# Kernel tuning notes

Hardware: AMD Instinct MI355X
Metric: run time of the kernel (lower is better)

## Reference

```python
import jax, jax.numpy as jnp
import numpy as np

B, T, C = 4, 2048, 1024
N_HEAD = 16
HEAD_DIM = C // N_HEAD


def setup_inputs() -> dict:
    key = jax.random.key(0)
    k1, k2, k3 = jax.random.split(key, 3)
    scale = 1.0 / np.sqrt(C)
    return {
        "x": jax.random.normal(k1, (B, T, C), dtype=jnp.float32),
        "W_attn": jax.random.normal(k2, (C, 3 * C), dtype=jnp.float32) * scale,
        "b_attn": jnp.zeros((3 * C,), dtype=jnp.float32),
        "W_proj": jax.random.normal(k3, (C, C), dtype=jnp.float32) * scale,
        "b_proj": jnp.zeros((C,), dtype=jnp.float32),
    }


def reference(x, W_attn, b_attn, W_proj, b_proj):
    Bt, Tt, Ct = x.shape
    qkv = x @ W_attn + b_attn                      # [B,T,3C]
    q, k, v = jnp.split(qkv, 3, axis=-1)
    # [B,T,C] -> [B,H,T,D]
    def heads(t):
        return t.reshape(Bt, Tt, N_HEAD, HEAD_DIM).transpose(0, 2, 1, 3)
    q, k, v = heads(q), heads(k), heads(v)
    att = jnp.einsum("bhqd,bhkd->bhqk", q, k) * (1.0 / np.sqrt(HEAD_DIM))
    causal = jnp.tril(jnp.ones((Tt, Tt), dtype=bool))
    att = jnp.where(causal, att, jnp.finfo(att.dtype).min)
    att = jax.nn.softmax(att, axis=-1)
    # dropout = 0.0 (eval mode): identity
    y = jnp.einsum("bhqk,bhkd->bhqd", att, v)      # [B,H,T,D]
    y = y.transpose(0, 2, 1, 3).reshape(Bt, Tt, Ct)
    return y @ W_proj + b_proj
```

## Files before the change

kernel.cpp:

```cpp
#include <hip/hip_runtime.h>
#include <hip/hip_bf16.h>
#include <cstdint>

#define B_SZ 4
#define T_SZ 2048
#define C_SZ 1024
#define H_SZ 16
#define D_SZ 64
#define BT_SZ (B_SZ * T_SZ)
#define C3_SZ (3 * C_SZ)
#define NKC (C_SZ / 32)

typedef __attribute__((ext_vector_type(8))) short bf16x8;
typedef __attribute__((ext_vector_type(4))) float f32x4;
typedef __attribute__((ext_vector_type(4))) unsigned short ushort4v;
typedef __attribute__((ext_vector_type(4))) unsigned int uint4v;

typedef __attribute__((address_space(3))) unsigned int lds_u32;
typedef __attribute__((address_space(1))) const unsigned int glb_u32;

__device__ __forceinline__ unsigned short f2bf(float f) {
  unsigned u = __builtin_bit_cast(unsigned, f);
  u += 0x7fffu + ((u >> 16) & 1u);
  return (unsigned short)(u >> 16);
}

__device__ __forceinline__ unsigned packbf2(float lo, float hi) {
  return __builtin_amdgcn_perm(__builtin_bit_cast(unsigned, hi),
                               __builtin_bit_cast(unsigned, lo), 0x07060302u);
}

__device__ __forceinline__ void gll16(const unsigned short* g,
                                      unsigned short* l) {
  __builtin_amdgcn_global_load_lds((glb_u32*)g, (lds_u32*)l, 16, 0, 0);
}


__device__ __forceinline__ void pack_x_task(const float* __restrict__ x,
                                            unsigned short* __restrict__ Af,
                                            int task, int lane) {
  const int quad = lane >> 4, n = lane & 15;
  const int tb = task >> 5, kc = task & 31;
  const float* src = x + (size_t)(tb * 16 + n) * C_SZ + kc * 32 + quad * 8;
  float4 a = *(const float4*)src;
  float4 b = *(const float4*)(src + 4);
  ushort4v o0, o1;
  o0[0] = f2bf(a.x); o0[1] = f2bf(a.y); o0[2] = f2bf(a.z); o0[3] = f2bf(a.w);
  o1[0] = f2bf(b.x); o1[1] = f2bf(b.y); o1[2] = f2bf(b.z); o1[3] = f2bf(b.w);
  unsigned short* dst = Af + ((size_t)((tb * NKC + kc) * 4 + quad) * 16 + n) * 8;
  *(ushort4v*)dst = o0;
  *(ushort4v*)(dst + 4) = o1;
}

__device__ __forceinline__ void pack_w_task(const float* __restrict__ W,
                                            unsigned short* __restrict__ Wb,
                                            int N, int task, int lane) {
  const int quad = lane >> 4, n = lane & 15;
  const int nt = task >> 5, kc = task & 31;
  const int col = nt * 16 + n;
  const int k0 = kc * 32 + quad * 8;
  ushort4v o0, o1;
#pragma unroll
  for (int i = 0; i < 4; ++i) o0[i] = f2bf(W[(size_t)(k0 + i) * N + col]);
#pragma unroll
  for (int i = 0; i < 4; ++i) o1[i] = f2bf(W[(size_t)(k0 + 4 + i) * N + col]);
  unsigned short* dst = Wb + ((size_t)((nt * NKC + kc) * 4 + quad) * 16 + n) * 8;
  *(ushort4v*)dst = o0;
  *(ushort4v*)(dst + 4) = o1;
}

__global__ __launch_bounds__(256) void pack_all(
    const float* __restrict__ x, const float* __restrict__ Wa,
    const float* __restrict__ Wp, unsigned short* __restrict__ Af,
    unsigned short* __restrict__ Wab, unsigned short* __restrict__ Wpb) {
  const int bx = blockIdx.x;
  const int sub = threadIdx.x >> 6;
  const int lane = threadIdx.x & 63;
  if (bx < 4096) {
    pack_x_task(x, Af, bx * 4 + sub, lane);
  } else if (bx < 4096 + 1536) {
    pack_w_task(Wa, Wab, C3_SZ, (bx - 4096) * 4 + sub, lane);
  } else {
    pack_w_task(Wp, Wpb, C_SZ, (bx - 5632) * 4 + sub, lane);
  }
}

__device__ __forceinline__ void gemm128_mainloop(
    const unsigned short* __restrict__ A, const unsigned short* __restrict__ B,
    int tbB, int ntB, unsigned short* smem, f32x4 acc[4][4]) {
  const int tid = threadIdx.x;
  const int w = tid >> 6, lane = tid & 63;
  const int quad = lane >> 4, n = lane & 15;
  const int wr = w >> 1, wc = w & 1;
  unsigned short* smemA = smem;
  unsigned short* smemB = smem + 8192;

  for (int kc0 = 0; kc0 < NKC; kc0 += 2) {
#pragma unroll
    for (int i2 = 0; i2 < 2; ++i2) {
      const int i = 2 * w + i2;
      const unsigned short* gA =
          A + ((size_t)(tbB + i) * NKC + kc0) * 512 + lane * 8;
      const unsigned short* gB =
          B + ((size_t)(ntB + i) * NKC + kc0) * 512 + lane * 8;
      gll16(gA, smemA + i * 1024);
      gll16(gA + 512, smemA + i * 1024 + 512);
      gll16(gB, smemB + i * 1024);
      gll16(gB + 512, smemB + i * 1024 + 512);
    }
    __syncthreads();
#pragma unroll
    for (int kcl = 0; kcl < 2; ++kcl) {
      bf16x8 af[4], bfr[4];
#pragma unroll
      for (int m = 0; m < 4; ++m)
        af[m] = *(const bf16x8*)(smemA + (wr * 4 + m) * 1024 +
                                 (kcl * 4 + quad) * 128 + n * 8);
#pragma unroll
      for (int nn = 0; nn < 4; ++nn)
        bfr[nn] = *(const bf16x8*)(smemB + (wc * 4 + nn) * 1024 +
                                   (kcl * 4 + quad) * 128 + n * 8);
#pragma unroll
      for (int m = 0; m < 4; ++m)
#pragma unroll
        for (int nn = 0; nn < 4; ++nn)
          acc[m][nn] = __builtin_amdgcn_mfma_f32_16x16x32_bf16(
              af[m], bfr[nn], acc[m][nn], 0, 0, 0);
    }
    __syncthreads();
  }
}

__global__ __launch_bounds__(256) void qkv_mfma(
    const unsigned short* __restrict__ Af, const unsigned short* __restrict__ Wab,
    const float* __restrict__ bias, unsigned short* __restrict__ Qf,
    unsigned short* __restrict__ Kf, unsigned short* __restrict__ Vf,
    int by0) {
  __shared__ unsigned short smem[16384];
  const int tid = threadIdx.x;
  const int w = tid >> 6, lane = tid & 63;
  const int quad = lane >> 4, n = lane & 15;
  const int wr = w >> 1, wc = w & 1;
  const int f = blockIdx.x;
  const int xcd = f & 7, i = f >> 3;
  const int by = by0 + xcd * 4 + (i / 24);
  const int bx = i % 24;
  f32x4 acc[4][4];
#pragma unroll
  for (int m = 0; m < 4; ++m)
#pragma unroll
    for (int nn = 0; nn < 4; ++nn) acc[m][nn] = (f32x4){0.f, 0.f, 0.f, 0.f};

  gemm128_mainloop(Af, Wab, by * 8, bx * 8, smem, acc);

  const int cb = bx * 128 + wc * 64;
  const int which = cb >> 10;
  const int h = (cb & 1023) >> 6;
  const int gr0 = by * 128 + wr * 64;
  const int b = gr0 >> 11;
  const int t0 = gr0 & 2047;
  const size_t bhoff = (size_t)(b * H_SZ + h) * (T_SZ * D_SZ);
  float bfl[4];
#pragma unroll
  for (int nn = 0; nn < 4; ++nn) bfl[nn] = bias[cb + nn * 16 + n];

  if (which < 2) {
    unsigned short* dst = ((which == 0) ? Qf : Kf) + bhoff;
    const float scl = (which == 0) ? 0.18033688f : 1.0f;
#pragma unroll
    for (int m = 0; m < 4; ++m) {
      const int tb = (t0 + m * 16) >> 4;
#pragma unroll
      for (int nn = 0; nn < 4; ++nn) {
        const int dc = nn >> 1;
        const int qd = (nn & 1) * 2 + (n >> 3);
        const int jq = n & 7;
#pragma unroll
        for (int r = 0; r < 4; ++r) {
          const int nq = quad * 4 + r;
          dst[((size_t)((tb * 2 + dc) * 4 + qd)) * 128 + nq * 8 + jq] =
              f2bf((acc[m][nn][r] + bfl[nn]) * scl);
        }
      }
    }
  } else {
    unsigned short* dst = Vf + bhoff;
    const int gb0 = t0 >> 5;
#pragma unroll
    for (int m = 0; m < 4; ++m) {
      const int gb = gb0 + (m >> 1);
#pragma unroll
      for (int nn = 0; nn < 4; ++nn) {
        ushort4v o;
#pragma unroll
        for (int r = 0; r < 4; ++r) o[r] = f2bf(acc[m][nn][r] + bfl[nn]);
        *(ushort4v*)(dst + ((size_t)((gb * 4 + nn) * 4 + quad)) * 128 +
                     n * 8 + (m & 1) * 4) = o;
      }
    }
  }
}

__global__ __launch_bounds__(256) void proj_mfma(
    const unsigned short* __restrict__ Yf, const unsigned short* __restrict__ Wpb,
    const float* __restrict__ bias, float* __restrict__ out) {
  __shared__ unsigned short smem[16384];
  const int tid = threadIdx.x;
  const int w = tid >> 6, lane = tid & 63;
  const int quad = lane >> 4, n = lane & 15;
  const int wr = w >> 1, wc = w & 1;
  const int f = blockIdx.x;
  const int xcd = f & 7, i = f >> 3;
  const int by = xcd * 8 + (i / 8);
  const int bx = i % 8;
  f32x4 acc[4][4];
#pragma unroll
  for (int m = 0; m < 4; ++m)
#pragma unroll
    for (int nn = 0; nn < 4; ++nn) acc[m][nn] = (f32x4){0.f, 0.f, 0.f, 0.f};

  gemm128_mainloop(Yf, Wpb, by * 8, bx * 8, smem, acc);

  const int cb = bx * 128 + wc * 64;
  const int gr0 = by * 128 + wr * 64;
  float bfl[4];
#pragma unroll
  for (int nn = 0; nn < 4; ++nn) bfl[nn] = bias[cb + nn * 16 + n];
#pragma unroll
  for (int m = 0; m < 4; ++m)
#pragma unroll
    for (int nn = 0; nn < 4; ++nn)
#pragma unroll
      for (int r = 0; r < 4; ++r)
        out[(size_t)(gr0 + m * 16 + quad * 4 + r) * C_SZ + cb + nn * 16 + n] =
            acc[m][nn][r] + bfl[nn];
}

__global__ __launch_bounds__(64) void attn_mfma(
    const unsigned short* __restrict__ Qf,
    const unsigned short* __restrict__ Kf,
    const unsigned short* __restrict__ Vf, unsigned short* __restrict__ Yf) {
  const int lane = threadIdx.x;
  const int quad = lane >> 4;
  const int n = lane & 15;
  const int bx = blockIdx.x;
  const int qt = 31 - (bx >> 6);
  const int bh = bx & 63;
  const int b = bh >> 4, h = bh & 15;
  const int wq0 = qt * 64;
  const size_t bhoff = (size_t)bh * (T_SZ * D_SZ);
  const bf16x8* Qp = (const bf16x8*)(Qf + bhoff);
  const bf16x8* Kp = (const bf16x8*)(Kf + bhoff);
  const bf16x8* Vp = (const bf16x8*)(Vf + bhoff);

  bf16x8 qfr[4][2];
#pragma unroll
  for (int m = 0; m < 4; ++m) {
    const int tb = (wq0 >> 4) + m;
#pragma unroll
    for (int dc = 0; dc < 2; ++dc)
      qfr[m][dc] = Qp[((tb * 2 + dc) * 4 + quad) * 16 + n];
  }

  bf16x8 kfr[4][2], vfr[2][4];
  f32x4 O[4][4];
  f32x4 ls[4];
#pragma unroll
  for (int m = 0; m < 4; ++m) {
    ls[m] = (f32x4){0.f, 0.f, 0.f, 0.f};
#pragma unroll
    for (int dv = 0; dv < 4; ++dv) O[m][dv] = (f32x4){0.f, 0.f, 0.f, 0.f};
  }

#pragma unroll
  for (int s = 0; s < 4; ++s) {
    kfr[s][0] = Kp[((s * 2 + 0) * 4 + quad) * 16 + n];
    kfr[s][1] = Kp[((s * 2 + 1) * 4 + quad) * 16 + n];
  }
#pragma unroll
  for (int g = 0; g < 2; ++g)
#pragma unroll
    for (int dv = 0; dv < 4; ++dv)
      vfr[g][dv] = Vp[((g * 4 + dv) * 4 + quad) * 16 + n];

  for (int kt = 0; kt < qt; ++kt) {
#pragma unroll
    for (int m = 0; m < 4; ++m) {
      f32x4 st[4];
#pragma unroll
      for (int s = 0; s < 4; ++s) {
        f32x4 z = {0.f, 0.f, 0.f, 0.f};
        z = __builtin_amdgcn_mfma_f32_16x16x32_bf16(kfr[s][0], qfr[m][0], z, 0, 0, 0);
        z = __builtin_amdgcn_mfma_f32_16x16x32_bf16(kfr[s][1], qfr[m][1], z, 0, 0, 0);
        st[s] = z;
      }
      if (m == 3) {
        const int tb0 = (kt + 1) * 4;
#pragma unroll
        for (int s = 0; s < 4; ++s) {
          kfr[s][0] = Kp[(((tb0 + s) * 2 + 0) * 4 + quad) * 16 + n];
          kfr[s][1] = Kp[(((tb0 + s) * 2 + 1) * 4 + quad) * 16 + n];
        }
      }
      uint4v pw[2];
#pragma unroll
      for (int s = 0; s < 4; ++s) {
        float pr[4];
#pragma unroll
        for (int r = 0; r < 4; ++r) {
          pr[r] = __builtin_amdgcn_exp2f(st[s][r]);
          ls[m][r] += pr[r];
        }
        pw[s >> 1][(s & 1) * 2 + 0] = packbf2(pr[0], pr[1]);
        pw[s >> 1][(s & 1) * 2 + 1] = packbf2(pr[2], pr[3]);
      }
#pragma unroll
      for (int g = 0; g < 2; ++g) {
        const bf16x8 pg = __builtin_bit_cast(bf16x8, pw[g]);
#pragma unroll
        for (int dv = 0; dv < 4; ++dv)
          O[m][dv] = __builtin_amdgcn_mfma_f32_16x16x32_bf16(
              pg, vfr[g][dv], O[m][dv], 0, 0, 0);
      }
      if (m == 3) {
        const int gb0 = (kt + 1) * 2;
#pragma unroll
        for (int g = 0; g < 2; ++g)
#pragma unroll
          for (int dv = 0; dv < 4; ++dv)
            vfr[g][dv] = Vp[(((gb0 + g) * 4 + dv) * 4 + quad) * 16 + n];
      }
    }
  }

  {
#pragma unroll
    for (int m = 0; m < 4; ++m) {
      f32x4 st[4];
#pragma unroll
      for (int s = 0; s < 4; ++s) {
        f32x4 z = {0.f, 0.f, 0.f, 0.f};
        if (s <= m) {
          z = __builtin_amdgcn_mfma_f32_16x16x32_bf16(kfr[s][0], qfr[m][0], z, 0, 0, 0);
          z = __builtin_amdgcn_mfma_f32_16x16x32_bf16(kfr[s][1], qfr[m][1], z, 0, 0, 0);
        }
        st[s] = z;
      }
      uint4v pw[2] = {(uint4v){0, 0, 0, 0}, (uint4v){0, 0, 0, 0}};
#pragma unroll
      for (int s = 0; s < 4; ++s) {
        if (s <= m) {
          float pr[4];
#pragma unroll
          for (int r = 0; r < 4; ++r) {
            float v = st[s][r];
            if (s == m && quad * 4 + r > n) v = -1e30f;
            pr[r] = __builtin_amdgcn_exp2f(v);
            ls[m][r] += pr[r];
          }
          pw[s >> 1][(s & 1) * 2 + 0] = packbf2(pr[0], pr[1]);
          pw[s >> 1][(s & 1) * 2 + 1] = packbf2(pr[2], pr[3]);
        }
      }
#pragma unroll
      for (int g = 0; g < 2; ++g) {
        if (g * 2 <= m) {
          const bf16x8 pg = __builtin_bit_cast(bf16x8, pw[g]);
#pragma unroll
          for (int dv = 0; dv < 4; ++dv)
            O[m][dv] = __builtin_amdgcn_mfma_f32_16x16x32_bf16(
                pg, vfr[g][dv], O[m][dv], 0, 0, 0);
        }
      }
    }
  }

#pragma unroll
  for (int m = 0; m < 4; ++m) {
    float lt = ls[m][0] + ls[m][1] + ls[m][2] + ls[m][3];
    lt += __shfl_xor(lt, 16);
    lt += __shfl_xor(lt, 32);
    const float inv = 1.0f / lt;
    float iv[4];
#pragma unroll
    for (int r = 0; r < 4; ++r) iv[r] = __shfl(inv, quad * 4 + r);
    const int tb = (b * T_SZ + wq0 + m * 16) >> 4;
#pragma unroll
    for (int dv = 0; dv < 4; ++dv) {
      const int kc = h * 2 + (dv >> 1);
      const int qa = (dv & 1) * 2 + (n >> 3);
      const int ja = n & 7;
#pragma unroll
      for (int r = 0; r < 4; ++r) {
        const int na = quad * 4 + r;
        Yf[((size_t)((tb * NKC + kc) * 4 + qa)) * 128 + na * 8 + ja] =
            f2bf(O[m][dv][r] * iv[r]);
      }
    }
  }
}

extern "C" void kernel_launch(void* const* d_in, const int* in_sizes, int n_in,
                              void* d_out, int out_size, void* d_ws,
                              size_t ws_size, hipStream_t stream) {
  const float* x = (const float*)d_in[0];
  const float* W_attn = (const float*)d_in[1];
  const float* b_attn = (const float*)d_in[2];
  const float* W_proj = (const float*)d_in[3];
  const float* b_proj = (const float*)d_in[4];
  float* out = (float*)d_out;

  const size_t perbf = (size_t)B_SZ * H_SZ * T_SZ * D_SZ;
  unsigned short* Af = (unsigned short*)d_ws;
  unsigned short* Wab = Af + (size_t)BT_SZ * C_SZ;
  unsigned short* Wpb = Wab + (size_t)C_SZ * C3_SZ;
  unsigned short* Qf = Wpb + (size_t)C_SZ * C_SZ;
  unsigned short* Kf = Qf + perbf;
  unsigned short* Vf = Kf + perbf;
  unsigned short* Yf = Vf + perbf;

  pack_all<<<6144, 256, 0, stream>>>(x, W_attn, W_proj, Af, Wab, Wpb);
  qkv_mfma<<<768, 256, 0, stream>>>(Af, Wab, b_attn, Qf, Kf, Vf, 0);
  qkv_mfma<<<768, 256, 0, stream>>>(Af, Wab, b_attn, Qf, Kf, Vf, 32);
  attn_mfma<<<dim3(32 * B_SZ * H_SZ), 64, 0, stream>>>(Qf, Kf, Vf, Yf);
  proj_mfma<<<512, 256, 0, stream>>>(Yf, Wpb, b_proj, out);
}
```

Measured before the change: 240.8 us.

## Pair causal query tiles per attention block and merge QKV launches

```diff
diff --git a/kernel.cpp b/kernel.cpp
--- a/kernel.cpp
+++ b/kernel.cpp
@@ -134,8 +134,7 @@
 __global__ __launch_bounds__(256) void qkv_mfma(
     const unsigned short* __restrict__ Af, const unsigned short* __restrict__ Wab,
     const float* __restrict__ bias, unsigned short* __restrict__ Qf,
-    unsigned short* __restrict__ Kf, unsigned short* __restrict__ Vf,
-    int by0) {
+    unsigned short* __restrict__ Kf, unsigned short* __restrict__ Vf) {
   __shared__ unsigned short smem[16384];
   const int tid = threadIdx.x;
   const int w = tid >> 6, lane = tid & 63;
@@ -143,7 +142,7 @@
   const int wr = w >> 1, wc = w & 1;
   const int f = blockIdx.x;
   const int xcd = f & 7, i = f >> 3;
-  const int by = by0 + xcd * 4 + (i / 24);
+  const int by = xcd * 8 + (i / 24);
   const int bx = i % 24;
   f32x4 acc[4][4];
 #pragma unroll
@@ -244,160 +243,172 @@
   const int quad = lane >> 4;
   const int n = lane & 15;
   const int bx = blockIdx.x;
-  const int qt = 31 - (bx >> 6);
+  const int p = bx >> 6;
   const int bh = bx & 63;
   const int b = bh >> 4, h = bh & 15;
-  const int wq0 = qt * 64;
   const size_t bhoff = (size_t)bh * (T_SZ * D_SZ);
   const bf16x8* Qp = (const bf16x8*)(Qf + bhoff);
   const bf16x8* Kp = (const bf16x8*)(Kf + bhoff);
   const bf16x8* Vp = (const bf16x8*)(Vf + bhoff);
 
-  bf16x8 qfr[4][2];
-#pragma unroll
-  for (int m = 0; m < 4; ++m) {
-    const int tb = (wq0 >> 4) + m;
-#pragma unroll
-    for (int dc = 0; dc < 2; ++dc)
-      qfr[m][dc] = Qp[((tb * 2 + dc) * 4 + quad) * 16 + n];
-  }
-
-  bf16x8 kfr[4][2], vfr[2][4];
-  f32x4 O[4][4];
-  f32x4 ls[4];
-#pragma unroll
-  for (int m = 0; m < 4; ++m) {
-    ls[m] = (f32x4){0.f, 0.f, 0.f, 0.f};
-#pragma unroll
-    for (int dv = 0; dv < 4; ++dv) O[m][dv] = (f32x4){0.f, 0.f, 0.f, 0.f};
-  }
-
-#pragma unroll
-  for (int s = 0; s < 4; ++s) {
-    kfr[s][0] = Kp[((s * 2 + 0) * 4 + quad) * 16 + n];
-    kfr[s][1] = Kp[((s * 2 + 1) * 4 + quad) * 16 + n];
-  }
-#pragma unroll
-  for (int g = 0; g < 2; ++g)
-#pragma unroll
-    for (int dv = 0; dv < 4; ++dv)
-      vfr[g][dv] = Vp[((g * 4 + dv) * 4 + quad) * 16 + n];
-
-  for (int kt = 0; kt < qt; ++kt) {
+  auto process = [&](int qt) {
+    const int wq0 = qt * 64;
+    bf16x8 qfr[4][2];
 #pragma unroll
     for (int m = 0; m < 4; ++m) {
-      f32x4 st[4];
+      const int tb = (wq0 >> 4) + m;
+#pragma unroll
+      for (int dc = 0; dc < 2; ++dc)
+        qfr[m][dc] = Qp[((tb * 2 + dc) * 4 + quad) * 16 + n];
+    }
+    f32x4 O[4][4];
+    f32x4 ls[4];
+#pragma unroll
+    for (int m = 0; m < 4; ++m) {
+      ls[m] = (f32x4){0.f, 0.f, 0.f, 0.f};
+#pragma unroll
+      for (int dv = 0; dv < 4; ++dv) O[m][dv] = (f32x4){0.f, 0.f, 0.f, 0.f};
+    }
+    bf16x8 k0[4][2], k1[4][2], v0[2][4], v1[2][4];
+#pragma unroll
+    for (int s = 0; s < 4; ++s) {
+      k0[s][0] = Kp[((s * 2 + 0) * 4 + quad) * 16 + n];
+      k0[s][1] = Kp[((s * 2 + 1) * 4 + quad) * 16 + n];
+    }
+#pragma unroll
+    for (int g = 0; g < 2; ++g)
+#pragma unroll
+      for (int dv = 0; dv < 4; ++dv)
+        v0[g][dv] = Vp[((g * 4 + dv) * 4 + quad) * 16 + n];
+
+    auto fulltile = [&](int kt, bf16x8 (&kc)[4][2], bf16x8 (&vc)[2][4],
+                        bf16x8 (&kn)[4][2], bf16x8 (&vn)[2][4]) {
+      const int tb0 = (kt + 1) * 4;
 #pragma unroll
       for (int s = 0; s < 4; ++s) {
-        f32x4 z = {0.f, 0.f, 0.f, 0.f};
-        z = __builtin_amdgcn_mfma_f32_16x16x32_bf16(kfr[s][0], qfr[m][0], z, 0, 0, 0);
-        z = __builtin_amdgcn_mfma_f32_16x16x32_bf16(kfr[s][1], qfr[m][1], z, 0, 0, 0);
-        st[s] = z;
-      }
-      if (m == 3) {
-        const int tb0 = (kt + 1) * 4;
+        kn[s][0] = Kp[(((tb0 + s) * 2 + 0) * 4 + quad) * 16 + n];
+        kn[s][1] = Kp[(((tb0 + s) * 2 + 1) * 4 + quad) * 16 + n];
+      }
+      const int gb0 = (kt + 1) * 2;
+#pragma unroll
+      for (int g = 0; g < 2; ++g)
+#pragma unroll
+        for (int dv = 0; dv < 4; ++dv)
+          vn[g][dv] = Vp[(((gb0 + g) * 4 + dv) * 4 + quad) * 16 + n];
+#pragma unroll
+      for (int m = 0; m < 4; ++m) {
+        f32x4 st[4];
 #pragma unroll
         for (int s = 0; s < 4; ++s) {
-          kfr[s][0] = Kp[(((tb0 + s) * 2 + 0) * 4 + quad) * 16 + n];
-          kfr[s][1] = Kp[(((tb0 + s) * 2 + 1) * 4 + quad) * 16 + n];
-        }
-      }
-      uint4v pw[2];
-#pragma unroll
-      for (int s = 0; s < 4; ++s) {
-        float pr[4];
-#pragma unroll
-        for (int r = 0; r < 4; ++r) {
-          pr[r] = __builtin_amdgcn_exp2f(st[s][r]);
-          ls[m][r] += pr[r];
-        }
-        pw[s >> 1][(s & 1) * 2 + 0] = packbf2(pr[0], pr[1]);
-        pw[s >> 1][(s & 1) * 2 + 1] = packbf2(pr[2], pr[3]);
-      }
-#pragma unroll
-      for (int g = 0; g < 2; ++g) {
-        const bf16x8 pg = __builtin_bit_cast(bf16x8, pw[g]);
-#pragma unroll
-        for (int dv = 0; dv < 4; ++dv)
-          O[m][dv] = __builtin_amdgcn_mfma_f32_16x16x32_bf16(
-              pg, vfr[g][dv], O[m][dv], 0, 0, 0);
-      }
-      if (m == 3) {
-        const int gb0 = (kt + 1) * 2;
-#pragma unroll
-        for (int g = 0; g < 2; ++g)
-#pragma unroll
-          for (int dv = 0; dv < 4; ++dv)
-            vfr[g][dv] = Vp[(((gb0 + g) * 4 + dv) * 4 + quad) * 16 + n];
-      }
-    }
-  }
-
-  {
-#pragma unroll
-    for (int m = 0; m < 4; ++m) {
-      f32x4 st[4];
-#pragma unroll
-      for (int s = 0; s < 4; ++s) {
-        f32x4 z = {0.f, 0.f, 0.f, 0.f};
-        if (s <= m) {
-          z = __builtin_amdgcn_mfma_f32_16x16x32_bf16(kfr[s][0], qfr[m][0], z, 0, 0, 0);
-          z = __builtin_amdgcn_mfma_f32_16x16x32_bf16(kfr[s][1], qfr[m][1], z, 0, 0, 0);
-        }
-        st[s] = z;
-      }
-      uint4v pw[2] = {(uint4v){0, 0, 0, 0}, (uint4v){0, 0, 0, 0}};
-#pragma unroll
-      for (int s = 0; s < 4; ++s) {
-        if (s <= m) {
+          f32x4 z = {0.f, 0.f, 0.f, 0.f};
+          z = __builtin_amdgcn_mfma_f32_16x16x32_bf16(kc[s][0], qfr[m][0], z, 0, 0, 0);
+          z = __builtin_amdgcn_mfma_f32_16x16x32_bf16(kc[s][1], qfr[m][1], z, 0, 0, 0);
+          st[s] = z;
+        }
+        uint4v pw[2];
+#pragma unroll
+        for (int s = 0; s < 4; ++s) {
           float pr[4];
 #pragma unroll
           for (int r = 0; r < 4; ++r) {
-            float v = st[s][r];
-            if (s == m && quad * 4 + r > n) v = -1e30f;
-            pr[r] = __builtin_amdgcn_exp2f(v);
+            pr[r] = __builtin_amdgcn_exp2f(st[s][r]);
             ls[m][r] += pr[r];
           }
           pw[s >> 1][(s & 1) * 2 + 0] = packbf2(pr[0], pr[1]);
           pw[s >> 1][(s & 1) * 2 + 1] = packbf2(pr[2], pr[3]);
         }
-      }
-#pragma unroll
-      for (int g = 0; g < 2; ++g) {
-        if (g * 2 <= m) {
+#pragma unroll
+        for (int g = 0; g < 2; ++g) {
           const bf16x8 pg = __builtin_bit_cast(bf16x8, pw[g]);
 #pragma unroll
           for (int dv = 0; dv < 4; ++dv)
             O[m][dv] = __builtin_amdgcn_mfma_f32_16x16x32_bf16(
-                pg, vfr[g][dv], O[m][dv], 0, 0, 0);
-        }
-      }
-    }
-  }
-
-#pragma unroll
-  for (int m = 0; m < 4; ++m) {
-    float lt = ls[m][0] + ls[m][1] + ls[m][2] + ls[m][3];
-    lt += __shfl_xor(lt, 16);
-    lt += __shfl_xor(lt, 32);
-    const float inv = 1.0f / lt;
-    float iv[4];
-#pragma unroll
-    for (int r = 0; r < 4; ++r) iv[r] = __shfl(inv, quad * 4 + r);
-    const int tb = (b * T_SZ + wq0 + m * 16) >> 4;
-#pragma unroll
-    for (int dv = 0; dv < 4; ++dv) {
-      const int kc = h * 2 + (dv >> 1);
-      const int qa = (dv & 1) * 2 + (n >> 3);
-      const int ja = n & 7;
-#pragma unroll
-      for (int r = 0; r < 4; ++r) {
-        const int na = quad * 4 + r;
-        Yf[((size_t)((tb * NKC + kc) * 4 + qa)) * 128 + na * 8 + ja] =
-            f2bf(O[m][dv][r] * iv[r]);
-      }
-    }
-  }
+                pg, vc[g][dv], O[m][dv], 0, 0, 0);
+        }
+      }
+    };
+
+    auto diagtile = [&](bf16x8 (&kc)[4][2], bf16x8 (&vc)[2][4]) {
+#pragma unroll
+      for (int m = 0; m < 4; ++m) {
+        f32x4 st[4];
+#pragma unroll
+        for (int s = 0; s < 4; ++s) {
+          f32x4 z = {0.f, 0.f, 0.f, 0.f};
+          if (s <= m) {
+            z = __builtin_amdgcn_mfma_f32_16x16x32_bf16(kc[s][0], qfr[m][0], z, 0, 0, 0);
+            z = __builtin_amdgcn_mfma_f32_16x16x32_bf16(kc[s][1], qfr[m][1], z, 0, 0, 0);
+          }
+          st[s] = z;
+        }
+        uint4v pw[2] = {(uint4v){0, 0, 0, 0}, (uint4v){0, 0, 0, 0}};
+#pragma unroll
+        for (int s = 0; s < 4; ++s) {
+          if (s <= m) {
+            float pr[4];
+#pragma unroll
+            for (int r = 0; r < 4; ++r) {
+              float v = st[s][r];
+              if (s == m && quad * 4 + r > n) v = -1e30f;
+              pr[r] = __builtin_amdgcn_exp2f(v);
+              ls[m][r] += pr[r];
+            }
+            pw[s >> 1][(s & 1) * 2 + 0] = packbf2(pr[0], pr[1]);
+            pw[s >> 1][(s & 1) * 2 + 1] = packbf2(pr[2], pr[3]);
+          }
+        }
+#pragma unroll
+        for (int g = 0; g < 2; ++g) {
+          if (g * 2 <= m) {
+            const bf16x8 pg = __builtin_bit_cast(bf16x8, pw[g]);
+#pragma unroll
+            for (int dv = 0; dv < 4; ++dv)
+              O[m][dv] = __builtin_amdgcn_mfma_f32_16x16x32_bf16(
+                  pg, vc[g][dv], O[m][dv], 0, 0, 0);
+          }
+        }
+      }
+    };
+
+    int k2 = 0;
+    for (; k2 + 2 <= qt; k2 += 2) {
+      fulltile(k2, k0, v0, k1, v1);
+      fulltile(k2 + 1, k1, v1, k0, v0);
+    }
+    if (qt & 1) {
+      fulltile(qt - 1, k0, v0, k1, v1);
+      diagtile(k1, v1);
+    } else {
+      diagtile(k0, v0);
+    }
+
+#pragma unroll
+    for (int m = 0; m < 4; ++m) {
+      float lt = ls[m][0] + ls[m][1] + ls[m][2] + ls[m][3];
+      lt += __shfl_xor(lt, 16);
+      lt += __shfl_xor(lt, 32);
+      const float inv = 1.0f / lt;
+      float iv[4];
+#pragma unroll
+      for (int r = 0; r < 4; ++r) iv[r] = __shfl(inv, quad * 4 + r);
+      const int tb = (b * T_SZ + wq0 + m * 16) >> 4;
+#pragma unroll
+      for (int dv = 0; dv < 4; ++dv) {
+        const int kc = h * 2 + (dv >> 1);
+        const int qa = (dv & 1) * 2 + (n >> 3);
+        const int ja = n & 7;
+#pragma unroll
+        for (int r = 0; r < 4; ++r) {
+          const int na = quad * 4 + r;
+          Yf[((size_t)((tb * NKC + kc) * 4 + qa)) * 128 + na * 8 + ja] =
+              f2bf(O[m][dv][r] * iv[r]);
+        }
+      }
+    }
+  };
+
+  process(31 - p);
+  process(p);
 }
 
 extern "C" void kernel_launch(void* const* d_in, const int* in_sizes, int n_in,
@@ -420,8 +431,7 @@
   unsigned short* Yf = Vf + perbf;
 
   pack_all<<<6144, 256, 0, stream>>>(x, W_attn, W_proj, Af, Wab, Wpb);
-  qkv_mfma<<<768, 256, 0, stream>>>(Af, Wab, b_attn, Qf, Kf, Vf, 0);
-  qkv_mfma<<<768, 256, 0, stream>>>(Af, Wab, b_attn, Qf, Kf, Vf, 32);
-  attn_mfma<<<dim3(32 * B_SZ * H_SZ), 64, 0, stream>>>(Qf, Kf, Vf, Yf);
+  qkv_mfma<<<1536, 256, 0, stream>>>(Af, Wab, b_attn, Qf, Kf, Vf);
+  attn_mfma<<<dim3(16 * B_SZ * H_SZ), 64, 0, stream>>>(Qf, Kf, Vf, Yf);
   proj_mfma<<<512, 256, 0, stream>>>(Yf, Wpb, b_proj, out);
 }
```

After: 222.0 us (median of 2 runs). 7.8% less time.
